# Performance work log

Hardware: AMD Instinct MI355X
Metric: run time of the kernel (lower is better)

Reference implementation:

```python
import jax, jax.numpy as jnp
import numpy as np

N = 50000      # nodes
E = 800000     # edges
IN = 16        # in_channels
H = 64         # hidden_dim
ED = 8         # edge_in_channels


def _sage(x, src, dst, Wl, Wr, b):
    # PyG SAGEConv (mean aggr): out = lin_l(mean_{j->i} x_j) + lin_r(x_i)
    agg = jax.ops.segment_sum(x[src], dst, num_segments=N)          # [N, F]
    cnt = jax.ops.segment_sum(jnp.ones((src.shape[0], 1), x.dtype), dst, num_segments=N)
    mean = agg / jnp.maximum(cnt, 1.0)
    return mean @ Wl + x @ Wr + b


def setup_inputs() -> dict:
    key = jax.random.key(0)
    ks = jax.random.split(key, 16)
    d = {}
    d['x'] = jax.random.normal(ks[0], (N, IN), dtype=jnp.float32)
    d['edge_index'] = jax.random.randint(ks[1], (2, E), 0, N, dtype=jnp.int32)
    d['edge_attr'] = jax.random.normal(ks[2], (E, ED), dtype=jnp.float32)
    def lin(k, fi, fo):
        s = 1.0 / np.sqrt(fi)
        return jax.random.uniform(k, (fi, fo), jnp.float32, -s, s)
    # SAGE conv params
    d['W1l'] = lin(ks[3], IN, H); d['W1r'] = lin(ks[4], IN, H); d['b1'] = jnp.zeros((H,), jnp.float32)
    d['W2l'] = lin(ks[5], H, H);  d['W2r'] = lin(ks[6], H, H);  d['b2'] = jnp.zeros((H,), jnp.float32)
    d['W3l'] = lin(ks[7], H, H);  d['W3r'] = lin(ks[8], H, H);  d['b3'] = jnp.zeros((H,), jnp.float32)
    # edge MLP: (2H+ED) -> H -> H//2 -> 1
    d['Wm1'] = lin(ks[9], 2 * H + ED, H); d['bm1'] = jnp.zeros((H,), jnp.float32)
    d['Wm2'] = lin(ks[10], H, H // 2);    d['bm2'] = jnp.zeros((H // 2,), jnp.float32)
    d['Wm3'] = lin(ks[11], H // 2, 1);    d['bm3'] = jnp.zeros((1,), jnp.float32)
    return d


def reference(x, edge_index, edge_attr, W1l, W1r, b1, W2l, W2r, b2, W3l, W3r, b3,
              Wm1, bm1, Wm2, bm2, Wm3, bm3):
    src, dst = edge_index[0], edge_index[1]
    h = jax.nn.relu(_sage(x, src, dst, W1l, W1r, b1))   # dropout: eval mode -> identity
    h = jax.nn.relu(_sage(h, src, dst, W2l, W2r, b2))
    h = jax.nn.relu(_sage(h, src, dst, W3l, W3r, b3))
    edge_feat = jnp.concatenate([h[src], h[dst], edge_attr], axis=1)  # [E, 2H+ED]
    z = jax.nn.relu(edge_feat @ Wm1 + bm1)
    z = jax.nn.relu(z @ Wm2 + bm2)
    logits = (z @ Wm3 + bm3).squeeze(-1)                # [E]
    return logits
```

## Files before the change

### kernel.cpp

```cpp
#include <hip/hip_runtime.h>


__global__ __launch_bounds__(256) void hist_kernel(const int* __restrict__ ei, int E,
                                                   int* __restrict__ cnt) {
    int e = blockIdx.x * blockDim.x + threadIdx.x;
    if (e < E) atomicAdd(&cnt[ei[E + e]], 1);
}

__global__ __launch_bounds__(1024) void scan_kernel(const int* __restrict__ cnt,
                                                    int* __restrict__ rowptr, int N) {
    __shared__ int sums[1024];
    int t = threadIdx.x;
    int chunk = (N + 1023) >> 10;
    int start = t * chunk;
    int end = min(start + chunk, N);
    int s = 0;
    for (int i = start; i < end; ++i) s += cnt[i];
    sums[t] = s;
    __syncthreads();
    for (int off = 1; off < 1024; off <<= 1) {
        int v = (t >= off) ? sums[t - off] : 0;
        __syncthreads();
        sums[t] += v;
        __syncthreads();
    }
    int run = (t == 0) ? 0 : sums[t - 1];
    if (t == 0) rowptr[0] = 0;
    for (int i = start; i < end; ++i) { run += cnt[i]; rowptr[i + 1] = run; }
}

__global__ __launch_bounds__(256) void fill_kernel(const int* __restrict__ ei, int E,
                                                   const int* __restrict__ rowptr,
                                                   int* __restrict__ cursor,
                                                   int2* __restrict__ sd,
                                                   int* __restrict__ eid) {
    int e = blockIdx.x * blockDim.x + threadIdx.x;
    if (e >= E) return;
    int s = ei[e], d = ei[E + e];
    int p = rowptr[d] + atomicAdd(&cursor[d], 1);
    sd[p] = make_int2(s, d);
    eid[p] = e;
}

__global__ __launch_bounds__(256) void sage16_kernel(
        const float* __restrict__ x, const int* __restrict__ rowptr,
        const int2* __restrict__ sd, const float* __restrict__ Wl,
        const float* __restrict__ Wr, const float* __restrict__ b,
        float* __restrict__ out, int N) {
    int lane = threadIdx.x & 63;
    int wid  = (blockIdx.x * blockDim.x + threadIdx.x) >> 6;
    if (wid >= N) return;
    int f = lane & 15, g = lane >> 4;
    int s0 = rowptr[wid], s1 = rowptr[wid + 1];
    float acc0 = 0.f, acc1 = 0.f;
    int j = s0 + g;
    for (; j + 4 < s1; j += 8) {
        int c0 = sd[j].x, c1 = sd[j + 4].x;
        acc0 += x[(size_t)c0 * 16 + f];
        acc1 += x[(size_t)c1 * 16 + f];
    }
    if (j < s1) acc0 += x[(size_t)sd[j].x * 16 + f];
    float acc = acc0 + acc1;
    acc += __shfl_xor(acc, 16);
    acc += __shfl_xor(acc, 32);
    float inv  = 1.0f / fmaxf((float)(s1 - s0), 1.0f);
    float mean = acc * inv;
    float xi   = x[(size_t)wid * 16 + f];
    float o = b[lane];
    #pragma unroll
    for (int ff = 0; ff < 16; ++ff) {
        float m  = __shfl(mean, ff);
        float xv = __shfl(xi, ff);
        o += m * Wl[ff * 64 + lane];
        o += xv * Wr[ff * 64 + lane];
    }
    out[(size_t)wid * 64 + lane] = fmaxf(o, 0.f);
}

__global__ __launch_bounds__(256) void gather_mean_kernel(
        const float* __restrict__ hin, const int* __restrict__ rowptr,
        const int2* __restrict__ sd, float* __restrict__ m, int N) {
    int lane = threadIdx.x & 63;
    int wid  = (blockIdx.x * blockDim.x + threadIdx.x) >> 6;
    if (wid >= N) return;
    int s0 = rowptr[wid], s1 = rowptr[wid + 1];
    float a0 = 0.f, a1 = 0.f, a2 = 0.f, a3 = 0.f;
    float a4 = 0.f, a5 = 0.f, a6 = 0.f, a7 = 0.f;
    int j = s0;
    for (; j + 8 <= s1; j += 8) {
        int c0 = sd[j].x,     c1 = sd[j + 1].x, c2 = sd[j + 2].x, c3 = sd[j + 3].x;
        int c4 = sd[j + 4].x, c5 = sd[j + 5].x, c6 = sd[j + 6].x, c7 = sd[j + 7].x;
        a0 += hin[(size_t)c0 * 64 + lane];
        a1 += hin[(size_t)c1 * 64 + lane];
        a2 += hin[(size_t)c2 * 64 + lane];
        a3 += hin[(size_t)c3 * 64 + lane];
        a4 += hin[(size_t)c4 * 64 + lane];
        a5 += hin[(size_t)c5 * 64 + lane];
        a6 += hin[(size_t)c6 * 64 + lane];
        a7 += hin[(size_t)c7 * 64 + lane];
    }
    for (; j < s1; ++j) a0 += hin[(size_t)sd[j].x * 64 + lane];
    float s = ((a0 + a1) + (a2 + a3)) + ((a4 + a5) + (a6 + a7));
    m[(size_t)wid * 64 + lane] = s / fmaxf((float)(s1 - s0), 1.0f);
}

__global__ __launch_bounds__(64) void linear64_kernel(
        const float* __restrict__ m, const float* __restrict__ h,
        const float* __restrict__ Wl, const float* __restrict__ Wr,
        const float* __restrict__ b, float* __restrict__ out, int N) {
    __shared__ float tile[64 * 132];
    int lane = threadIdx.x;
    int base = blockIdx.x * 64;
    for (int n = 0; n < 64; ++n) {
        int i = base + n;
        float mv = 0.f, hv = 0.f;
        if (i < N) { mv = m[(size_t)i * 64 + lane]; hv = h[(size_t)i * 64 + lane]; }
        tile[n * 132 + lane]      = mv;
        tile[n * 132 + 64 + lane] = hv;
    }
    __syncthreads();
    float y[64];
    #pragma unroll
    for (int c = 0; c < 64; ++c) y[c] = b[c];
    for (int it = 0; it < 16; ++it) {
        float4 z = *(const float4*)&tile[lane * 132 + it * 4];
        #pragma unroll
        for (int q = 0; q < 4; ++q) {
            float zv = q == 0 ? z.x : q == 1 ? z.y : q == 2 ? z.z : z.w;
            int ff = it * 4 + q;
            #pragma unroll
            for (int c = 0; c < 64; ++c) y[c] += zv * Wl[ff * 64 + c];
        }
    }
    for (int it = 0; it < 16; ++it) {
        float4 z = *(const float4*)&tile[lane * 132 + 64 + it * 4];
        #pragma unroll
        for (int q = 0; q < 4; ++q) {
            float zv = q == 0 ? z.x : q == 1 ? z.y : q == 2 ? z.z : z.w;
            int ff = it * 4 + q;
            #pragma unroll
            for (int c = 0; c < 64; ++c) y[c] += zv * Wr[ff * 64 + c];
        }
    }
    __syncthreads();
    #pragma unroll
    for (int c = 0; c < 64; ++c) tile[lane * 65 + c] = fmaxf(y[c], 0.f);
    __syncthreads();
    for (int n = 0; n < 64; ++n) {
        int i = base + n;
        if (i < N) out[(size_t)i * 64 + lane] = tile[n * 65 + lane];
    }
}

__global__ __launch_bounds__(64) void linear64_ab_kernel(
        const float* __restrict__ m, const float* __restrict__ h,
        const float* __restrict__ Wl, const float* __restrict__ Wr,
        const float* __restrict__ b, const float* __restrict__ Wm1,
        const float* __restrict__ bm1, float* __restrict__ A,
        float* __restrict__ Bf, int N) {
    __shared__ float tile[64 * 132];
    int lane = threadIdx.x;
    int base = blockIdx.x * 64;
    for (int n = 0; n < 64; ++n) {
        int i = base + n;
        float mv = 0.f, hv = 0.f;
        if (i < N) { mv = m[(size_t)i * 64 + lane]; hv = h[(size_t)i * 64 + lane]; }
        tile[n * 132 + lane]      = mv;
        tile[n * 132 + 64 + lane] = hv;
    }
    __syncthreads();
    float h3[64];
    #pragma unroll
    for (int c = 0; c < 64; ++c) h3[c] = b[c];
    for (int it = 0; it < 16; ++it) {
        float4 z = *(const float4*)&tile[lane * 132 + it * 4];
        #pragma unroll
        for (int q = 0; q < 4; ++q) {
            float zv = q == 0 ? z.x : q == 1 ? z.y : q == 2 ? z.z : z.w;
            int ff = it * 4 + q;
            #pragma unroll
            for (int c = 0; c < 64; ++c) h3[c] += zv * Wl[ff * 64 + c];
        }
    }
    for (int it = 0; it < 16; ++it) {
        float4 z = *(const float4*)&tile[lane * 132 + 64 + it * 4];
        #pragma unroll
        for (int q = 0; q < 4; ++q) {
            float zv = q == 0 ? z.x : q == 1 ? z.y : q == 2 ? z.z : z.w;
            int ff = it * 4 + q;
            #pragma unroll
            for (int c = 0; c < 64; ++c) h3[c] += zv * Wr[ff * 64 + c];
        }
    }
    #pragma unroll
    for (int c = 0; c < 64; ++c) h3[c] = fmaxf(h3[c], 0.f);
    {
        float yA[64];
        #pragma unroll
        for (int c = 0; c < 64; ++c) yA[c] = bm1[c];
        #pragma unroll
        for (int ff = 0; ff < 64; ++ff) {
            float zv = h3[ff];
            #pragma unroll
            for (int c = 0; c < 64; ++c) yA[c] += zv * Wm1[ff * 64 + c];
        }
        __syncthreads();
        #pragma unroll
        for (int c = 0; c < 64; ++c) tile[lane * 65 + c] = yA[c];
        __syncthreads();
        for (int n = 0; n < 64; ++n) {
            int i = base + n;
            if (i < N) A[(size_t)i * 64 + lane] = tile[n * 65 + lane];
        }
    }
    {
        float yB[64];
        #pragma unroll
        for (int c = 0; c < 64; ++c) yB[c] = 0.f;
        #pragma unroll
        for (int ff = 0; ff < 64; ++ff) {
            float zv = h3[ff];
            #pragma unroll
            for (int c = 0; c < 64; ++c) yB[c] += zv * Wm1[(64 + ff) * 64 + c];
        }
        __syncthreads();
        #pragma unroll
        for (int c = 0; c < 64; ++c) tile[lane * 65 + c] = yB[c];
        __syncthreads();
        for (int n = 0; n < 64; ++n) {
            int i = base + n;
            if (i < N) Bf[(size_t)i * 64 + lane] = tile[n * 65 + lane];
        }
    }
}

__global__ __launch_bounds__(64) void edge_kernel(
        const float* __restrict__ A, const float* __restrict__ Bf,
        const int2* __restrict__ sd, const int* __restrict__ eid,
        const float* __restrict__ attr,
        const float* __restrict__ Wm1, const float* __restrict__ Wm2,
        const float* __restrict__ bm2, const float* __restrict__ Wm3,
        const float* __restrict__ bm3, float* __restrict__ out, int E) {
    __shared__ float zt[64 * 68];
    int lane = threadIdx.x;
    int base = blockIdx.x * 64;
    float wmE[8];
    #pragma unroll
    for (int k = 0; k < 8; ++k) wmE[k] = Wm1[(128 + k) * 64 + lane];
    #pragma unroll 4
    for (int i = 0; i < 64; i += 2) {
        int e0 = base + i, e1 = base + i + 1;
        float z0 = 0.f, z1 = 0.f;
        if (e0 < E) {
            int2 p0 = sd[e0];
            int id0 = eid[e0];
            float v = A[(size_t)p0.x * 64 + lane] + Bf[(size_t)p0.y * 64 + lane];
            #pragma unroll
            for (int k = 0; k < 8; ++k) v += attr[(size_t)id0 * 8 + k] * wmE[k];
            z0 = fmaxf(v, 0.f);
        }
        if (e1 < E) {
            int2 p1 = sd[e1];
            int id1 = eid[e1];
            float v = A[(size_t)p1.x * 64 + lane] + Bf[(size_t)p1.y * 64 + lane];
            #pragma unroll
            for (int k = 0; k < 8; ++k) v += attr[(size_t)id1 * 8 + k] * wmE[k];
            z1 = fmaxf(v, 0.f);
        }
        zt[i * 68 + lane]       = z0;
        zt[(i + 1) * 68 + lane] = z1;
    }
    __syncthreads();
    float y[32];
    #pragma unroll
    for (int p = 0; p < 32; ++p) y[p] = bm2[p];
    for (int it = 0; it < 16; ++it) {
        float4 z = *(const float4*)&zt[lane * 68 + it * 4];
        #pragma unroll
        for (int q = 0; q < 4; ++q) {
            float zv = q == 0 ? z.x : q == 1 ? z.y : q == 2 ? z.z : z.w;
            int o = it * 4 + q;
            #pragma unroll
            for (int p = 0; p < 32; ++p) y[p] += zv * Wm2[o * 32 + p];
        }
    }
    float logit = bm3[0];
    #pragma unroll
    for (int p = 0; p < 32; ++p) logit += fmaxf(y[p], 0.f) * Wm3[p];
    int e = base + lane;
    if (e < E) out[eid[e]] = logit;
}

extern "C" void kernel_launch(void* const* d_in, const int* in_sizes, int n_in,
                              void* d_out, int out_size, void* d_ws, size_t ws_size,
                              hipStream_t stream) {
    const float* x    = (const float*)d_in[0];
    const int*   ei   = (const int*)d_in[1];
    const float* attr = (const float*)d_in[2];
    const float* W1l  = (const float*)d_in[3];
    const float* W1r  = (const float*)d_in[4];
    const float* b1   = (const float*)d_in[5];
    const float* W2l  = (const float*)d_in[6];
    const float* W2r  = (const float*)d_in[7];
    const float* b2   = (const float*)d_in[8];
    const float* W3l  = (const float*)d_in[9];
    const float* W3r  = (const float*)d_in[10];
    const float* b3   = (const float*)d_in[11];
    const float* Wm1  = (const float*)d_in[12];
    const float* bm1  = (const float*)d_in[13];
    const float* Wm2  = (const float*)d_in[14];
    const float* bm2  = (const float*)d_in[15];
    const float* Wm3  = (const float*)d_in[16];
    const float* bm3  = (const float*)d_in[17];
    float* out = (float*)d_out;

    const int N = in_sizes[0] / 16;
    const int E = in_sizes[1] / 2;

    char* ws = (char*)d_ws;
    size_t off = 0;
    int* cnt    = (int*)(ws + off); off += (size_t)N * 4;
    int* cursor = (int*)(ws + off); off += (size_t)N * 4;
    int* rowptr = (int*)(ws + off); off += (size_t)(N + 1) * 4;
    off = (off + 255) & ~(size_t)255;
    int2* sd    = (int2*)(ws + off); off += (size_t)E * 8;
    int* eid    = (int*)(ws + off);  off += (size_t)E * 4;
    off = (off + 255) & ~(size_t)255;
    float* h1 = (float*)(ws + off); off += (size_t)N * 64 * 4;
    float* h2 = (float*)(ws + off); off += (size_t)N * 64 * 4;
    float* mb = (float*)(ws + off); off += (size_t)N * 64 * 4;
    float* Bf = (float*)(ws + off); off += (size_t)N * 64 * 4;

    hipMemsetAsync(ws, 0, (size_t)N * 8, stream);

    const int TB = 256;
    int ebBlocks = (E + TB - 1) / TB;
    int nwBlocks = (N * 64 + TB - 1) / TB;
    int b64Nodes = (N + 63) / 64;
    int b64Edges = (E + 63) / 64;

    hist_kernel<<<ebBlocks, TB, 0, stream>>>(ei, E, cnt);
    scan_kernel<<<1, 1024, 0, stream>>>(cnt, rowptr, N);
    fill_kernel<<<ebBlocks, TB, 0, stream>>>(ei, E, rowptr, cursor, sd, eid);

    sage16_kernel<<<nwBlocks, TB, 0, stream>>>(x, rowptr, sd, W1l, W1r, b1, h1, N);

    gather_mean_kernel<<<nwBlocks, TB, 0, stream>>>(h1, rowptr, sd, mb, N);
    linear64_kernel<<<b64Nodes, 64, 0, stream>>>(mb, h1, W2l, W2r, b2, h2, N);

    gather_mean_kernel<<<nwBlocks, TB, 0, stream>>>(h2, rowptr, sd, mb, N);
    linear64_ab_kernel<<<b64Nodes, 64, 0, stream>>>(mb, h2, W3l, W3r, b3,
                                                    Wm1, bm1, h1, Bf, N);

    edge_kernel<<<b64Edges, 64, 0, stream>>>(h1, Bf, sd, eid, attr,
                                             Wm1, Wm2, bm2, Wm3, bm3, out, E);
}
```

Measured before the change: 815.2 us.

## Split node linear work across lanes and batch edge gathers in edge MLP

The node linear kernels now assign 8 lanes per node, each computing 8 output channels with vectorized weight loads. This replaces the 64-register-per-lane accumulators and the shared-memory transposes, and raises blocks to 256 threads. The edge kernel processes 64 edges in two batches of 32, issuing four edges' gathers at once with vectorized attr loads. The second-layer MLP is split across the two wave halves and combined with a cross-half shuffle. This aims to cut register pressure, raise occupancy and add memory-level parallelism, at the cost of redundant per-node row loads and an extra barrier per batch.

Measured after the change: 2.578 ms. +216.2%, slower.

```diff
diff --git a/kernel.cpp b/kernel.cpp
--- a/kernel.cpp
+++ b/kernel.cpp
@@ -1,5 +1,11 @@
 #include <hip/hip_runtime.h>
 
+
+__device__ __forceinline__ void fma8(float (&y)[8], float zv,
+                                     const float4& a, const float4& b) {
+    y[0] += zv * a.x; y[1] += zv * a.y; y[2] += zv * a.z; y[3] += zv * a.w;
+    y[4] += zv * b.x; y[5] += zv * b.y; y[6] += zv * b.z; y[7] += zv * b.w;
+}
 
 __global__ __launch_bounds__(256) void hist_kernel(const int* __restrict__ ei, int E,
                                                    int* __restrict__ cnt) {
@@ -104,133 +110,141 @@
     m[(size_t)wid * 64 + lane] = s / fmaxf((float)(s1 - s0), 1.0f);
 }
 
-__global__ __launch_bounds__(64) void linear64_kernel(
+__global__ __launch_bounds__(256) void linear64_kernel(
         const float* __restrict__ m, const float* __restrict__ h,
         const float* __restrict__ Wl, const float* __restrict__ Wr,
         const float* __restrict__ b, float* __restrict__ out, int N) {
-    __shared__ float tile[64 * 132];
-    int lane = threadIdx.x;
-    int base = blockIdx.x * 64;
-    for (int n = 0; n < 64; ++n) {
-        int i = base + n;
-        float mv = 0.f, hv = 0.f;
-        if (i < N) { mv = m[(size_t)i * 64 + lane]; hv = h[(size_t)i * 64 + lane]; }
-        tile[n * 132 + lane]      = mv;
-        tile[n * 132 + 64 + lane] = hv;
-    }
-    __syncthreads();
-    float y[64];
-    #pragma unroll
-    for (int c = 0; c < 64; ++c) y[c] = b[c];
-    for (int it = 0; it < 16; ++it) {
-        float4 z = *(const float4*)&tile[lane * 132 + it * 4];
-        #pragma unroll
-        for (int q = 0; q < 4; ++q) {
-            float zv = q == 0 ? z.x : q == 1 ? z.y : q == 2 ? z.z : z.w;
-            int ff = it * 4 + q;
-            #pragma unroll
-            for (int c = 0; c < 64; ++c) y[c] += zv * Wl[ff * 64 + c];
-        }
-    }
-    for (int it = 0; it < 16; ++it) {
-        float4 z = *(const float4*)&tile[lane * 132 + 64 + it * 4];
-        #pragma unroll
-        for (int q = 0; q < 4; ++q) {
-            float zv = q == 0 ? z.x : q == 1 ? z.y : q == 2 ? z.z : z.w;
-            int ff = it * 4 + q;
-            #pragma unroll
-            for (int c = 0; c < 64; ++c) y[c] += zv * Wr[ff * 64 + c];
-        }
-    }
-    __syncthreads();
-    #pragma unroll
-    for (int c = 0; c < 64; ++c) tile[lane * 65 + c] = fmaxf(y[c], 0.f);
-    __syncthreads();
-    for (int n = 0; n < 64; ++n) {
-        int i = base + n;
-        if (i < N) out[(size_t)i * 64 + lane] = tile[n * 65 + lane];
-    }
-}
-
-__global__ __launch_bounds__(64) void linear64_ab_kernel(
+    int lane = threadIdx.x & 63;
+    int wv   = threadIdx.x >> 6;
+    int ns   = lane >> 3, co = lane & 7;
+    int node = blockIdx.x * 32 + wv * 8 + ns;
+    int i    = min(node, N - 1);
+    float y[8];
+    {
+        float4 b0 = *(const float4*)&b[co * 8];
+        float4 b1 = *(const float4*)&b[co * 8 + 4];
+        y[0] = b0.x; y[1] = b0.y; y[2] = b0.z; y[3] = b0.w;
+        y[4] = b1.x; y[5] = b1.y; y[6] = b1.z; y[7] = b1.w;
+    }
+    const float* mrow = &m[(size_t)i * 64];
+    const float* hrow = &h[(size_t)i * 64];
+    for (int t = 0; t < 16; ++t) {
+        float4 z4 = *(const float4*)&mrow[t * 4];
+        #pragma unroll
+        for (int j = 0; j < 4; ++j) {
+            int ff = t * 4 + j;
+            float zv = j == 0 ? z4.x : j == 1 ? z4.y : j == 2 ? z4.z : z4.w;
+            float4 wa = *(const float4*)&Wl[ff * 64 + co * 8];
+            float4 wb = *(const float4*)&Wl[ff * 64 + co * 8 + 4];
+            fma8(y, zv, wa, wb);
+        }
+    }
+    for (int t = 0; t < 16; ++t) {
+        float4 z4 = *(const float4*)&hrow[t * 4];
+        #pragma unroll
+        for (int j = 0; j < 4; ++j) {
+            int ff = t * 4 + j;
+            float zv = j == 0 ? z4.x : j == 1 ? z4.y : j == 2 ? z4.z : z4.w;
+            float4 wa = *(const float4*)&Wr[ff * 64 + co * 8];
+            float4 wb = *(const float4*)&Wr[ff * 64 + co * 8 + 4];
+            fma8(y, zv, wa, wb);
+        }
+    }
+    if (node < N) {
+        float4 o0 = make_float4(fmaxf(y[0], 0.f), fmaxf(y[1], 0.f),
+                                fmaxf(y[2], 0.f), fmaxf(y[3], 0.f));
+        float4 o1 = make_float4(fmaxf(y[4], 0.f), fmaxf(y[5], 0.f),
+                                fmaxf(y[6], 0.f), fmaxf(y[7], 0.f));
+        *(float4*)&out[(size_t)node * 64 + co * 8]     = o0;
+        *(float4*)&out[(size_t)node * 64 + co * 8 + 4] = o1;
+    }
+}
+
+__global__ __launch_bounds__(256) void linear64_ab_kernel(
         const float* __restrict__ m, const float* __restrict__ h,
         const float* __restrict__ Wl, const float* __restrict__ Wr,
         const float* __restrict__ b, const float* __restrict__ Wm1,
         const float* __restrict__ bm1, float* __restrict__ A,
         float* __restrict__ Bf, int N) {
-    __shared__ float tile[64 * 132];
-    int lane = threadIdx.x;
-    int base = blockIdx.x * 64;
-    for (int n = 0; n < 64; ++n) {
-        int i = base + n;
-        float mv = 0.f, hv = 0.f;
-        if (i < N) { mv = m[(size_t)i * 64 + lane]; hv = h[(size_t)i * 64 + lane]; }
-        tile[n * 132 + lane]      = mv;
-        tile[n * 132 + 64 + lane] = hv;
+    __shared__ float xch[4][8 * 68];
+    int lane = threadIdx.x & 63;
+    int wv   = threadIdx.x >> 6;
+    int ns   = lane >> 3, co = lane & 7;
+    int node = blockIdx.x * 32 + wv * 8 + ns;
+    int i    = min(node, N - 1);
+    float y[8];
+    {
+        float4 b0 = *(const float4*)&b[co * 8];
+        float4 b1 = *(const float4*)&b[co * 8 + 4];
+        y[0] = b0.x; y[1] = b0.y; y[2] = b0.z; y[3] = b0.w;
+        y[4] = b1.x; y[5] = b1.y; y[6] = b1.z; y[7] = b1.w;
+    }
+    const float* mrow = &m[(size_t)i * 64];
+    const float* hrow = &h[(size_t)i * 64];
+    for (int t = 0; t < 16; ++t) {
+        float4 z4 = *(const float4*)&mrow[t * 4];
+        #pragma unroll
+        for (int j = 0; j < 4; ++j) {
+            int ff = t * 4 + j;
+            float zv = j == 0 ? z4.x : j == 1 ? z4.y : j == 2 ? z4.z : z4.w;
+            float4 wa = *(const float4*)&Wl[ff * 64 + co * 8];
+            float4 wb = *(const float4*)&Wl[ff * 64 + co * 8 + 4];
+            fma8(y, zv, wa, wb);
+        }
+    }
+    for (int t = 0; t < 16; ++t) {
+        float4 z4 = *(const float4*)&hrow[t * 4];
+        #pragma unroll
+        for (int j = 0; j < 4; ++j) {
+            int ff = t * 4 + j;
+            float zv = j == 0 ? z4.x : j == 1 ? z4.y : j == 2 ? z4.z : z4.w;
+            float4 wa = *(const float4*)&Wr[ff * 64 + co * 8];
+            float4 wb = *(const float4*)&Wr[ff * 64 + co * 8 + 4];
+            fma8(y, zv, wa, wb);
+        }
+    }
+    {
+        float4 h0 = make_float4(fmaxf(y[0], 0.f), fmaxf(y[1], 0.f),
+                                fmaxf(y[2], 0.f), fmaxf(y[3], 0.f));
+        float4 h1 = make_float4(fmaxf(y[4], 0.f), fmaxf(y[5], 0.f),
+                                fmaxf(y[6], 0.f), fmaxf(y[7], 0.f));
+        *(float4*)&xch[wv][ns * 68 + co * 8]     = h0;
+        *(float4*)&xch[wv][ns * 68 + co * 8 + 4] = h1;
     }
     __syncthreads();
-    float h3[64];
-    #pragma unroll
-    for (int c = 0; c < 64; ++c) h3[c] = b[c];
-    for (int it = 0; it < 16; ++it) {
-        float4 z = *(const float4*)&tile[lane * 132 + it * 4];
-        #pragma unroll
-        for (int q = 0; q < 4; ++q) {
-            float zv = q == 0 ? z.x : q == 1 ? z.y : q == 2 ? z.z : z.w;
-            int ff = it * 4 + q;
-            #pragma unroll
-            for (int c = 0; c < 64; ++c) h3[c] += zv * Wl[ff * 64 + c];
-        }
-    }
-    for (int it = 0; it < 16; ++it) {
-        float4 z = *(const float4*)&tile[lane * 132 + 64 + it * 4];
-        #pragma unroll
-        for (int q = 0; q < 4; ++q) {
-            float zv = q == 0 ? z.x : q == 1 ? z.y : q == 2 ? z.z : z.w;
-            int ff = it * 4 + q;
-            #pragma unroll
-            for (int c = 0; c < 64; ++c) h3[c] += zv * Wr[ff * 64 + c];
-        }
-    }
-    #pragma unroll
-    for (int c = 0; c < 64; ++c) h3[c] = fmaxf(h3[c], 0.f);
+    float yA[8], yB[8];
     {
-        float yA[64];
-        #pragma unroll
-        for (int c = 0; c < 64; ++c) yA[c] = bm1[c];
-        #pragma unroll
-        for (int ff = 0; ff < 64; ++ff) {
-            float zv = h3[ff];
-            #pragma unroll
-            for (int c = 0; c < 64; ++c) yA[c] += zv * Wm1[ff * 64 + c];
-        }
-        __syncthreads();
-        #pragma unroll
-        for (int c = 0; c < 64; ++c) tile[lane * 65 + c] = yA[c];
-        __syncthreads();
-        for (int n = 0; n < 64; ++n) {
-            int i = base + n;
-            if (i < N) A[(size_t)i * 64 + lane] = tile[n * 65 + lane];
-        }
-    }
-    {
-        float yB[64];
-        #pragma unroll
-        for (int c = 0; c < 64; ++c) yB[c] = 0.f;
-        #pragma unroll
-        for (int ff = 0; ff < 64; ++ff) {
-            float zv = h3[ff];
-            #pragma unroll
-            for (int c = 0; c < 64; ++c) yB[c] += zv * Wm1[(64 + ff) * 64 + c];
-        }
-        __syncthreads();
-        #pragma unroll
-        for (int c = 0; c < 64; ++c) tile[lane * 65 + c] = yB[c];
-        __syncthreads();
-        for (int n = 0; n < 64; ++n) {
-            int i = base + n;
-            if (i < N) Bf[(size_t)i * 64 + lane] = tile[n * 65 + lane];
-        }
+        float4 b0 = *(const float4*)&bm1[co * 8];
+        float4 b1 = *(const float4*)&bm1[co * 8 + 4];
+        yA[0] = b0.x; yA[1] = b0.y; yA[2] = b0.z; yA[3] = b0.w;
+        yA[4] = b1.x; yA[5] = b1.y; yA[6] = b1.z; yA[7] = b1.w;
+        #pragma unroll
+        for (int q = 0; q < 8; ++q) yB[q] = 0.f;
+    }
+    const float* zrow = &xch[wv][ns * 68];
+    for (int t = 0; t < 16; ++t) {
+        float4 z4 = *(const float4*)&zrow[t * 4];
+        #pragma unroll
+        for (int j = 0; j < 4; ++j) {
+            int ff = t * 4 + j;
+            float zv = j == 0 ? z4.x : j == 1 ? z4.y : j == 2 ? z4.z : z4.w;
+            float4 wa = *(const float4*)&Wm1[ff * 64 + co * 8];
+            float4 wb = *(const float4*)&Wm1[ff * 64 + co * 8 + 4];
+            fma8(yA, zv, wa, wb);
+            float4 va = *(const float4*)&Wm1[(64 + ff) * 64 + co * 8];
+            float4 vb = *(const float4*)&Wm1[(64 + ff) * 64 + co * 8 + 4];
+            fma8(yB, zv, va, vb);
+        }
+    }
+    if (node < N) {
+        *(float4*)&A[(size_t)node * 64 + co * 8] =
+            make_float4(yA[0], yA[1], yA[2], yA[3]);
+        *(float4*)&A[(size_t)node * 64 + co * 8 + 4] =
+            make_float4(yA[4], yA[5], yA[6], yA[7]);
+        *(float4*)&Bf[(size_t)node * 64 + co * 8] =
+            make_float4(yB[0], yB[1], yB[2], yB[3]);
+        *(float4*)&Bf[(size_t)node * 64 + co * 8 + 4] =
+            make_float4(yB[4], yB[5], yB[6], yB[7]);
     }
 }
 
@@ -241,54 +255,80 @@
         const float* __restrict__ Wm1, const float* __restrict__ Wm2,
         const float* __restrict__ bm2, const float* __restrict__ Wm3,
         const float* __restrict__ bm3, float* __restrict__ out, int E) {
-    __shared__ float zt[64 * 68];
+    __shared__ float zt[32 * 68];
     int lane = threadIdx.x;
     int base = blockIdx.x * 64;
     float wmE[8];
     #pragma unroll
     for (int k = 0; k < 8; ++k) wmE[k] = Wm1[(128 + k) * 64 + lane];
-    #pragma unroll 4
-    for (int i = 0; i < 64; i += 2) {
-        int e0 = base + i, e1 = base + i + 1;
-        float z0 = 0.f, z1 = 0.f;
-        if (e0 < E) {
-            int2 p0 = sd[e0];
-            int id0 = eid[e0];
-            float v = A[(size_t)p0.x * 64 + lane] + Bf[(size_t)p0.y * 64 + lane];
+    const float4* attr4 = (const float4*)attr;
+    int eh = lane & 31, hh = lane >> 5;
+    float bias3 = bm3[0];
+
+    for (int batch = 0; batch < 2; ++batch) {
+        int ebase = base + batch * 32;
+        for (int i = 0; i < 32; i += 4) {
+            int e0 = ebase + i;
+            int ec0 = min(e0,     E - 1), ec1 = min(e0 + 1, E - 1);
+            int ec2 = min(e0 + 2, E - 1), ec3 = min(e0 + 3, E - 1);
+            int2 p0 = sd[ec0], p1 = sd[ec1], p2 = sd[ec2], p3 = sd[ec3];
+            int id0 = eid[ec0], id1 = eid[ec1], id2 = eid[ec2], id3 = eid[ec3];
+            float a0 = A[(size_t)p0.x * 64 + lane];
+            float a1 = A[(size_t)p1.x * 64 + lane];
+            float a2 = A[(size_t)p2.x * 64 + lane];
+            float a3 = A[(size_t)p3.x * 64 + lane];
+            float v0 = Bf[(size_t)p0.y * 64 + lane];
+            float v1 = Bf[(size_t)p1.y * 64 + lane];
+            float v2 = Bf[(size_t)p2.y * 64 + lane];
+            float v3 = Bf[(size_t)p3.y * 64 + lane];
+            float4 q0a = attr4[(size_t)id0 * 2], q0b = attr4[(size_t)id0 * 2 + 1];
+            float4 q1a = attr4[(size_t)id1 * 2], q1b = attr4[(size_t)id1 * 2 + 1];
+            float4 q2a = attr4[(size_t)id2 * 2], q2b = attr4[(size_t)id2 * 2 + 1];
+            float4 q3a = attr4[(size_t)id3 * 2], q3b = attr4[(size_t)id3 * 2 + 1];
+            float z0 = a0 + v0 + q0a.x*wmE[0] + q0a.y*wmE[1] + q0a.z*wmE[2] + q0a.w*wmE[3]
+                               + q0b.x*wmE[4] + q0b.y*wmE[5] + q0b.z*wmE[6] + q0b.w*wmE[7];
+            float z1 = a1 + v1 + q1a.x*wmE[0] + q1a.y*wmE[1] + q1a.z*wmE[2] + q1a.w*wmE[3]
+                               + q1b.x*wmE[4] + q1b.y*wmE[5] + q1b.z*wmE[6] + q1b.w*wmE[7];
+            float z2 = a2 + v2 + q2a.x*wmE[0] + q2a.y*wmE[1] + q2a.z*wmE[2] + q2a.w*wmE[3]
+                               + q2b.x*wmE[4] + q2b.y*wmE[5] + q2b.z*wmE[6] + q2b.w*wmE[7];
+            float z3 = a3 + v3 + q3a.x*wmE[0] + q3a.y*wmE[1] + q3a.z*wmE[2] + q3a.w*wmE[3]
+                               + q3b.x*wmE[4] + q3b.y*wmE[5] + q3b.z*wmE[6] + q3b.w*wmE[7];
+            zt[(i + 0) * 68 + lane] = fmaxf(z0, 0.f);
+            zt[(i + 1) * 68 + lane] = fmaxf(z1, 0.f);
+            zt[(i + 2) * 68 + lane] = fmaxf(z2, 0.f);
+            zt[(i + 3) * 68 + lane] = fmaxf(z3, 0.f);
+        }
+        __syncthreads();
+        float y[32];
+        #pragma unroll
+        for (int p = 0; p < 32; ++p) y[p] = hh ? 0.f : bm2[p];
+        const float* zrow = &zt[eh * 68 + hh * 32];
+        #pragma unroll
+        for (int it = 0; it < 8; ++it) {
+            float4 z4 = *(const float4*)&zrow[it * 4];
             #pragma unroll
-            for (int k = 0; k < 8; ++k) v += attr[(size_t)id0 * 8 + k] * wmE[k];
-            z0 = fmaxf(v, 0.f);
-        }
-        if (e1 < E) {
-            int2 p1 = sd[e1];
-            int id1 = eid[e1];
-            float v = A[(size_t)p1.x * 64 + lane] + Bf[(size_t)p1.y * 64 + lane];
-            #pragma unroll
-            for (int k = 0; k < 8; ++k) v += attr[(size_t)id1 * 8 + k] * wmE[k];
-            z1 = fmaxf(v, 0.f);
-        }
-        zt[i * 68 + lane]       = z0;
-        zt[(i + 1) * 68 + lane] = z1;
-    }
-    __syncthreads();
-    float y[32];
-    #pragma unroll
-    for (int p = 0; p < 32; ++p) y[p] = bm2[p];
-    for (int it = 0; it < 16; ++it) {
-        float4 z = *(const float4*)&zt[lane * 68 + it * 4];
-        #pragma unroll
-        for (int q = 0; q < 4; ++q) {
-            float zv = q == 0 ? z.x : q == 1 ? z.y : q == 2 ? z.z : z.w;
-            int o = it * 4 + q;
-            #pragma unroll
-            for (int p = 0; p < 32; ++p) y[p] += zv * Wm2[o * 32 + p];
-        }
-    }
-    float logit = bm3[0];
-    #pragma unroll
-    for (int p = 0; p < 32; ++p) logit += fmaxf(y[p], 0.f) * Wm3[p];
-    int e = base + lane;
-    if (e < E) out[eid[e]] = logit;
+            for (int j = 0; j < 4; ++j) {
+                float zv = j == 0 ? z4.x : j == 1 ? z4.y : j == 2 ? z4.z : z4.w;
+                int o = hh * 32 + it * 4 + j;
+                #pragma unroll
+                for (int k = 0; k < 8; ++k) {
+                    float4 w = *(const float4*)&Wm2[o * 32 + k * 4];
+                    y[k * 4 + 0] += zv * w.x;
+                    y[k * 4 + 1] += zv * w.y;
+                    y[k * 4 + 2] += zv * w.z;
+                    y[k * 4 + 3] += zv * w.w;
+                }
+            }
+        }
+        #pragma unroll
+        for (int p = 0; p < 32; ++p) y[p] += __shfl_xor(y[p], 32);
+        float logit = bias3;
+        #pragma unroll
+        for (int p = 0; p < 32; ++p) logit += fmaxf(y[p], 0.f) * Wm3[p];
+        int e = ebase + eh;
+        if (hh == 0 && e < E) out[eid[e]] = logit;
+        __syncthreads();
+    }
 }
 
 extern "C" void kernel_launch(void* const* d_in, const int* in_sizes, int n_in,
@@ -334,10 +374,10 @@
     hipMemsetAsync(ws, 0, (size_t)N * 8, stream);
 
     const int TB = 256;
-    int ebBlocks = (E + TB - 1) / TB;
-    int nwBlocks = (N * 64 + TB - 1) / TB;
-    int b64Nodes = (N + 63) / 64;
-    int b64Edges = (E + 63) / 64;
+    int ebBlocks  = (E + TB - 1) / TB;
+    int nwBlocks  = (N * 64 + TB - 1) / TB;
+    int n32Blocks = (N + 31) / 32;
+    int b64Edges  = (E + 63) / 64;
 
     hist_kernel<<<ebBlocks, TB, 0, stream>>>(ei, E, cnt);
     scan_kernel<<<1, 1024, 0, stream>>>(cnt, rowptr, N);
@@ -346,11 +386,11 @@
     sage16_kernel<<<nwBlocks, TB, 0, stream>>>(x, rowptr, sd, W1l, W1r, b1, h1, N);
 
     gather_mean_kernel<<<nwBlocks, TB, 0, stream>>>(h1, rowptr, sd, mb, N);
-    linear64_kernel<<<b64Nodes, 64, 0, stream>>>(mb, h1, W2l, W2r, b2, h2, N);
+    linear64_kernel<<<n32Blocks, TB, 0, stream>>>(mb, h1, W2l, W2r, b2, h2, N);
 
     gather_mean_kernel<<<nwBlocks, TB, 0, stream>>>(h2, rowptr, sd, mb, N);
-    linear64_ab_kernel<<<b64Nodes, 64, 0, stream>>>(mb, h2, W3l, W3r, b3,
-                                                    Wm1, bm1, h1, Bf, N);
+    linear64_ab_kernel<<<n32Blocks, TB, 0, stream>>>(mb, h2, W3l, W3r, b3,
+                                                     Wm1, bm1, h1, Bf, N);
 
     edge_kernel<<<b64Edges, 64, 0, stream>>>(h1, Bf, sd, eid, attr,
                                              Wm1, Wm2, bm2, Wm3, bm3, out, E);
```
